# Kernel tuning notes

Hardware: AMD Instinct MI355X
Metric: run time of the kernel (lower is better)

## Reference

```python
import jax, jax.numpy as jnp
import numpy as np

N_NODES = 50000
N_EDGES = 800000
N_GRAPHS = 512
D_IN = 64
D_HID = 64
D_CLS = 128
LEAKY_SLOPE = 0.01


def _glorot(key, shape):
    fan_in, fan_out = shape[0], shape[1]
    lim = jnp.sqrt(6.0 / (fan_in + fan_out)).astype(jnp.float32)
    return jax.random.uniform(key, shape, jnp.float32, -lim, lim)


def setup_inputs() -> dict:
    key = jax.random.key(0)
    ks = jax.random.split(key, 16)
    x = jax.random.normal(ks[0], (N_NODES, D_IN), jnp.float32)
    edge_index = jax.random.randint(ks[1], (2, N_EDGES), 0, N_NODES, jnp.int32)
    batch = jnp.sort(jax.random.randint(ks[2], (N_NODES,), 0, N_GRAPHS, jnp.int32))
    return {
        'x': x,
        'W0': _glorot(ks[3], (D_IN, D_HID)), 'b0': jnp.zeros((D_HID,), jnp.float32),
        'W1': _glorot(ks[4], (D_HID, D_HID)), 'b1': jnp.zeros((D_HID,), jnp.float32),
        'W2': _glorot(ks[5], (D_HID, D_HID)), 'b2': jnp.zeros((D_HID,), jnp.float32),
        'lin1_w': _glorot(ks[6], (D_HID, D_CLS)), 'lin1_b': jnp.zeros((D_CLS,), jnp.float32),
        'lin2_w': _glorot(ks[7], (D_CLS, 1)), 'lin2_b': jnp.zeros((1,), jnp.float32),
        'fc_w': _glorot(ks[8], (1, 1)), 'fc_b': jnp.zeros((1,), jnp.float32),
        'edge_index': edge_index,
        'batch': batch,
    }


def _gcn_layer(h_in, W, b, src, dst, edge_norm, deg_inv):
    # GCNConv: linear transform, then symmetric-normalized aggregation with self-loops
    h = h_in @ W                                        # [N, D]
    msgs = h[src] * edge_norm[:, None]                  # gather + scale, [E, D]
    agg = jax.ops.segment_sum(msgs, dst, num_segments=N_NODES)  # scatter-add
    return agg + deg_inv[:, None] * h + b               # self-loop term + bias


def reference(x, W0, b0, W1, b1, W2, b2, lin1_w, lin1_b, lin2_w, lin2_b, fc_w, fc_b, edge_index, batch):
    src, dst = edge_index[0], edge_index[1]
    # degrees including self-loop (A + I)
    deg = jax.ops.segment_sum(jnp.ones((N_EDGES,), jnp.float32), dst, num_segments=N_NODES) + 1.0
    deg_inv_sqrt = jax.lax.rsqrt(deg)
    deg_inv = 1.0 / deg
    edge_norm = deg_inv_sqrt[src] * deg_inv_sqrt[dst]   # [E]

    h = _gcn_layer(x, W0, b0, src, dst, edge_norm, deg_inv)
    h = _gcn_layer(h, W1, b1, src, dst, edge_norm, deg_inv)
    h = _gcn_layer(h, W2, b2, src, dst, edge_norm, deg_inv)

    # global_mean_pool over graphs
    sums = jax.ops.segment_sum(h, batch, num_segments=N_GRAPHS)          # [G, D]
    counts = jax.ops.segment_sum(jnp.ones((N_NODES,), jnp.float32), batch, num_segments=N_GRAPHS)
    pooled = sums / jnp.maximum(counts, 1.0)[:, None]

    out = pooled @ lin1_w + lin1_b      # [G, cls_hidden]
    out = out @ lin2_w + lin2_b         # [G, 1]
    out = out @ fc_w + fc_b             # [G, 1]
    return jnp.where(out >= 0, out, LEAKY_SLOPE * out)  # LeakyReLU
```

## Files before the change

kernel.cpp:

```cpp
#include <hip/hip_runtime.h>
#include <math.h>

#define N_NODES 50000
#define N_EDGES 800000
#define N_GRAPHS 512
#define D 64
#define D_CLS 128
#define BNODES 128
#define NBUK 391
#define BSTRIDE 4096
#define PART_TILE 4096

typedef _Float16 h4 __attribute__((ext_vector_type(4)));
typedef float    f4 __attribute__((ext_vector_type(4)));

static inline int cdiv(int a, int b) { return (a + b - 1) / b; }


__global__ void k_binit(int* __restrict__ btail) {
    int b = blockIdx.x * blockDim.x + threadIdx.x;
    if (b < NBUK) btail[b] = b * BSTRIDE;
}


__global__ __launch_bounds__(256) void k_part(
        const int* __restrict__ src, const int* __restrict__ dst,
        int* __restrict__ btail, int* __restrict__ ebuf) {
    __shared__ int lcnt[NBUK];
    __shared__ int lbase[NBUK];
    int t = threadIdx.x;
    for (int i = t; i < NBUK; i += 256) lcnt[i] = 0;
    __syncthreads();

    int e0 = blockIdx.x * PART_TILE + t;
    int ent[16];
    int br[16];
    #pragma unroll
    for (int k = 0; k < 16; k++) {
        int e = e0 + k * 256;
        if (e < N_EDGES) {
            int d = dst[e];
            int b = d / BNODES;
            int r = atomicAdd(&lcnt[b], 1);
            ent[k] = src[e] | ((d & (BNODES - 1)) << 16);
            br[k] = (b << 16) | r;
        } else {
            br[k] = -1;
        }
    }
    __syncthreads();
    for (int i = t; i < NBUK; i += 256) {
        int c = lcnt[i];
        lbase[i] = c ? atomicAdd(&btail[i], c) : 0;
    }
    __syncthreads();
    #pragma unroll
    for (int k = 0; k < 16; k++) {
        if (br[k] >= 0) {
            int b = br[k] >> 16, r = br[k] & 0xFFFF;
            ebuf[lbase[b] + r] = ent[k];
        }
    }
}


__global__ __launch_bounds__(256) void k_build(
        const int* __restrict__ ebuf, const int* __restrict__ btail,
        int* __restrict__ rstart, int* __restrict__ rend,
        float* __restrict__ dis, int* __restrict__ col) {
    __shared__ int hist[BNODES];
    __shared__ int base[BNODES];
    __shared__ int cur[BNODES];
    int t = threadIdx.x;
    int b = blockIdx.x;
    int s = b * BSTRIDE;
    int e = btail[b];

    if (t < BNODES) { hist[t] = 0; cur[t] = 0; }
    __syncthreads();

    for (int i = s + t; i < e; i += 256)
        atomicAdd(&hist[(ebuf[i] >> 16) & (BNODES - 1)], 1);
    __syncthreads();

    if (t < BNODES) base[t] = hist[t];
    __syncthreads();
    for (int off = 1; off < BNODES; off <<= 1) {
        int x = 0;
        if (t < BNODES && t >= off) x = base[t - off];
        __syncthreads();
        if (t < BNODES) base[t] += x;
        __syncthreads();
    }
    if (t < BNODES) {
        int ex = base[t] - hist[t];
        base[t] = ex;
        int n = b * BNODES + t;
        if (n < N_NODES) {
            rstart[n] = s + ex;
            rend[n]   = s + ex + hist[t];
            dis[n] = rsqrtf((float)hist[t] + 1.0f);
        }
    }
    __syncthreads();

    for (int i = s + t; i < e; i += 256) {
        int v = ebuf[i];
        int d = (v >> 16) & (BNODES - 1);
        int pos = atomicAdd(&cur[d], 1);
        col[s + base[d] + pos] = v & 0xFFFF;
    }
}


#define XS_STRIDE 68

__global__ __launch_bounds__(256) void k_gemm_scale(
        const float* __restrict__ X, const float* __restrict__ W,
        const float* __restrict__ dis, _Float16* __restrict__ G16) {
    __shared__ float Xs[64 * XS_STRIDE];
    __shared__ float Ws[64 * 64];
    int n0 = blockIdx.x * 64;
    int t = threadIdx.x;

    {
        int base = t * 16;
        const float4* wsrc = (const float4*)(W + base);
        float4* wdst = (float4*)(Ws + base);
        wdst[0] = wsrc[0]; wdst[1] = wsrc[1]; wdst[2] = wsrc[2]; wdst[3] = wsrc[3];
    }
    {
        int row = t >> 2;
        int c0 = (t & 3) * 16;
        int grow = n0 + row;
        float4* xd = (float4*)(Xs + row * XS_STRIDE + c0);
        if (grow < N_NODES) {
            const float4* xp = (const float4*)(X + (size_t)grow * D + c0);
            xd[0] = xp[0]; xd[1] = xp[1]; xd[2] = xp[2]; xd[3] = xp[3];
        } else {
            float4 z = {0.f, 0.f, 0.f, 0.f};
            xd[0] = z; xd[1] = z; xd[2] = z; xd[3] = z;
        }
    }
    __syncthreads();

    int tc = t & 15, tr = t >> 4;
    int r0 = tr * 4, c0 = tc * 4;
    float acc[4][4] = {};
    #pragma unroll 4
    for (int k = 0; k < 64; k++) {
        float4 wv = *(const float4*)&Ws[k * 64 + c0];
        #pragma unroll
        for (int i = 0; i < 4; i++) {
            float xv = Xs[(r0 + i) * XS_STRIDE + k];
            acc[i][0] = fmaf(xv, wv.x, acc[i][0]);
            acc[i][1] = fmaf(xv, wv.y, acc[i][1]);
            acc[i][2] = fmaf(xv, wv.z, acc[i][2]);
            acc[i][3] = fmaf(xv, wv.w, acc[i][3]);
        }
    }
    #pragma unroll
    for (int i = 0; i < 4; i++) {
        int grow = n0 + r0 + i;
        if (grow < N_NODES) {
            float dsc = dis[grow];
            h4 o;
            o.x = (_Float16)(acc[i][0] * dsc);
            o.y = (_Float16)(acc[i][1] * dsc);
            o.z = (_Float16)(acc[i][2] * dsc);
            o.w = (_Float16)(acc[i][3] * dsc);
            *(h4*)&G16[(size_t)grow * D + c0] = o;
        }
    }
}


__global__ __launch_bounds__(256) void k_agg(
        const _Float16* __restrict__ G16, const int* __restrict__ rstart,
        const int* __restrict__ rend, const int* __restrict__ col,
        const float* __restrict__ dis, const float* __restrict__ bias,
        float* __restrict__ Out) {
    int t = threadIdx.x;
    int grp = t >> 4;
    int fl4 = (t & 15) * 4;
    int n = blockIdx.x * 16 + grp;

    int s = rstart[n], e = rend[n];
    f4 acc = __builtin_convertvector(*(const h4*)(G16 + (size_t)n * D + fl4), f4);

    for (int i = s; i < e; i += 8) {
        int i1 = i + 1, i2 = i + 2, i3 = i + 3;
        int i4 = i + 4, i5 = i + 5, i6 = i + 6, i7 = i + 7;
        int c0 = col[i];
        int c1 = col[i1 < e ? i1 : i];
        int c2 = col[i2 < e ? i2 : i];
        int c3 = col[i3 < e ? i3 : i];
        int c4 = col[i4 < e ? i4 : i];
        int c5 = col[i5 < e ? i5 : i];
        int c6 = col[i6 < e ? i6 : i];
        int c7 = col[i7 < e ? i7 : i];
        float f1 = (i1 < e) ? 1.f : 0.f;
        float f2 = (i2 < e) ? 1.f : 0.f;
        float f3 = (i3 < e) ? 1.f : 0.f;
        float f4_ = (i4 < e) ? 1.f : 0.f;
        float f5 = (i5 < e) ? 1.f : 0.f;
        float f6 = (i6 < e) ? 1.f : 0.f;
        float f7 = (i7 < e) ? 1.f : 0.f;
        f4 g0 = __builtin_convertvector(*(const h4*)(G16 + (size_t)c0 * D + fl4), f4);
        f4 g1 = __builtin_convertvector(*(const h4*)(G16 + (size_t)c1 * D + fl4), f4);
        f4 g2 = __builtin_convertvector(*(const h4*)(G16 + (size_t)c2 * D + fl4), f4);
        f4 g3 = __builtin_convertvector(*(const h4*)(G16 + (size_t)c3 * D + fl4), f4);
        f4 g4 = __builtin_convertvector(*(const h4*)(G16 + (size_t)c4 * D + fl4), f4);
        f4 g5 = __builtin_convertvector(*(const h4*)(G16 + (size_t)c5 * D + fl4), f4);
        f4 g6 = __builtin_convertvector(*(const h4*)(G16 + (size_t)c6 * D + fl4), f4);
        f4 g7 = __builtin_convertvector(*(const h4*)(G16 + (size_t)c7 * D + fl4), f4);
        acc += g0;
        acc += f1 * g1;
        acc += f2 * g2;
        acc += f3 * g3;
        acc += f4_ * g4;
        acc += f5 * g5;
        acc += f6 * g6;
        acc += f7 * g7;
    }

    float dsc = dis[n];
    f4 bv = *(const f4*)(bias + fl4);
    f4 o = dsc * acc + bv;
    *(f4*)(Out + (size_t)n * D + fl4) = o;
}


__device__ __forceinline__ int lower_bound_batch(const int* batch, int g) {
    int lo = 0, hi = N_NODES;
    while (lo < hi) {
        int mid = (lo + hi) >> 1;
        if (batch[mid] < g) lo = mid + 1; else hi = mid;
    }
    return lo;
}

__global__ __launch_bounds__(256) void k_pool(
        const float* __restrict__ H, const int* __restrict__ batch,
        float* __restrict__ P) {
    int g = blockIdx.x * 4 + (threadIdx.x >> 6);
    if (g >= N_GRAPHS) return;
    int lane = threadIdx.x & 63;
    int es  = lane >> 4;
    int fg4 = (lane & 15) * 4;
    int s = lower_bound_batch(batch, g);
    int e = lower_bound_batch(batch, g + 1);
    float4 acc = {0.f, 0.f, 0.f, 0.f};
    for (int r = s + es; r < e; r += 4) {
        float4 h = *(const float4*)(H + (size_t)r * D + fg4);
        acc.x += h.x; acc.y += h.y; acc.z += h.z; acc.w += h.w;
    }
    #pragma unroll
    for (int m = 16; m < 64; m <<= 1) {
        acc.x += __shfl_xor(acc.x, m, 64);
        acc.y += __shfl_xor(acc.y, m, 64);
        acc.z += __shfl_xor(acc.z, m, 64);
        acc.w += __shfl_xor(acc.w, m, 64);
    }
    int cntr = e - s;
    float inv = 1.0f / (float)(cntr > 0 ? cntr : 1);
    if (es == 0) {
        float4 o;
        o.x = acc.x * inv; o.y = acc.y * inv; o.z = acc.z * inv; o.w = acc.w * inv;
        *(float4*)(P + g * D + fg4) = o;
    }
}


__global__ __launch_bounds__(128) void k_mlp(
        const float* __restrict__ P,
        const float* __restrict__ w1, const float* __restrict__ b1,
        const float* __restrict__ w2, const float* __restrict__ b2,
        const float* __restrict__ fcw, const float* __restrict__ fcb,
        float* __restrict__ out) {
    __shared__ float ps[64];
    __shared__ float red[128];
    int g = blockIdx.x, t = threadIdx.x;
    if (t < 64) ps[t] = P[g * D + t];
    __syncthreads();
    float acc = b1[t];
    #pragma unroll
    for (int k = 0; k < 64; k++) acc = fmaf(ps[k], w1[k * D_CLS + t], acc);
    red[t] = acc * w2[t];
    __syncthreads();
    for (int s2 = 64; s2 > 0; s2 >>= 1) {
        if (t < s2) red[t] += red[t + s2];
        __syncthreads();
    }
    if (t == 0) {
        float o = red[0] + b2[0];
        o = fmaf(o, fcw[0], fcb[0]);
        out[g] = (o >= 0.f) ? o : 0.01f * o;
    }
}


extern "C" void kernel_launch(void* const* d_in, const int* in_sizes, int n_in,
                              void* d_out, int out_size, void* d_ws, size_t ws_size,
                              hipStream_t stream) {
    const float* x   = (const float*)d_in[0];
    const float* W0  = (const float*)d_in[1];
    const float* b0  = (const float*)d_in[2];
    const float* W1  = (const float*)d_in[3];
    const float* b1  = (const float*)d_in[4];
    const float* W2  = (const float*)d_in[5];
    const float* b2  = (const float*)d_in[6];
    const float* l1w = (const float*)d_in[7];
    const float* l1b = (const float*)d_in[8];
    const float* l2w = (const float*)d_in[9];
    const float* l2b = (const float*)d_in[10];
    const float* fcw = (const float*)d_in[11];
    const float* fcb = (const float*)d_in[12];
    const int* eidx  = (const int*)d_in[13];
    const int* batch = (const int*)d_in[14];
    const int* src = eidx;
    const int* dst = eidx + N_EDGES;

    char* ws = (char*)d_ws;
    size_t off = 0;
    auto alloc = [&](size_t bytes) -> void* {
        off = (off + 255) & ~(size_t)255;
        void* p = ws + off;
        off += bytes;
        return p;
    };

    int*   rstart = (int*)  alloc(N_NODES * sizeof(int));
    int*   rend   = (int*)  alloc(N_NODES * sizeof(int));
    int*   btail  = (int*)  alloc(NBUK * sizeof(int));
    int*   ebuf   = (int*)  alloc((size_t)NBUK * BSTRIDE * sizeof(int));
    int*   col    = (int*)  alloc((size_t)NBUK * BSTRIDE * sizeof(int));
    float* dis    = (float*)alloc(N_NODES * sizeof(float));
    _Float16* G16 = (_Float16*)alloc((size_t)N_NODES * D * sizeof(_Float16));
    float* bufB   = (float*)alloc((size_t)N_NODES * D * sizeof(float));
    float* bufC   = (float*)alloc((size_t)N_NODES * D * sizeof(float));
    float* pooled = (float*)alloc((size_t)N_GRAPHS * D * sizeof(float));

    const int nbPart = cdiv(N_EDGES, PART_TILE);

    k_binit<<<cdiv(NBUK, 256), 256, 0, stream>>>(btail);
    k_part<<<nbPart, 256, 0, stream>>>(src, dst, btail, ebuf);
    k_build<<<NBUK, 256, 0, stream>>>(ebuf, btail, rstart, rend, dis, col);

    const int nbGemm = cdiv(N_NODES, 64);
    const int nbAgg  = cdiv(N_NODES, 16);

    k_gemm_scale<<<nbGemm, 256, 0, stream>>>(x, W0, dis, G16);
    k_agg<<<nbAgg, 256, 0, stream>>>(G16, rstart, rend, col, dis, b0, bufB);
    k_gemm_scale<<<nbGemm, 256, 0, stream>>>(bufB, W1, dis, G16);
    k_agg<<<nbAgg, 256, 0, stream>>>(G16, rstart, rend, col, dis, b1, bufC);
    k_gemm_scale<<<nbGemm, 256, 0, stream>>>(bufC, W2, dis, G16);
    k_agg<<<nbAgg, 256, 0, stream>>>(G16, rstart, rend, col, dis, b2, bufB);

    k_pool<<<cdiv(N_GRAPHS, 4), 256, 0, stream>>>(bufB, batch, pooled);
    k_mlp<<<N_GRAPHS, 128, 0, stream>>>(pooled, l1w, l1b, l2w, l2b, fcw, fcb,
                                        (float*)d_out);
}
```

Measured before the change: 143.7 us.

## Store intermediate node features in fp16, fuse pooling into MLP, stage CSR build in LDS

Aggregation outputs are now written as fp16 and the next GEMM reads fp16 input, which halves the intermediate activation traffic between layers. Mean pooling is fused into the MLP kernel, removing one launch and the pooled buffer. The CSR build kernel stages its bucket in shared memory so the edge buffer is read from global memory once instead of twice. The cost is extra fp16 rounding of the hidden activations, and a pooling step now spread over 512 blocks of only 128 threads with narrow scalar loads.

Result: slower. 148.6 us (+3.4%).

```diff
diff --git a/kernel.cpp b/kernel.cpp
--- a/kernel.cpp
+++ b/kernel.cpp
@@ -68,19 +68,23 @@
         const int* __restrict__ ebuf, const int* __restrict__ btail,
         int* __restrict__ rstart, int* __restrict__ rend,
         float* __restrict__ dis, int* __restrict__ col) {
+    __shared__ int stage[BSTRIDE];
     __shared__ int hist[BNODES];
     __shared__ int base[BNODES];
     __shared__ int cur[BNODES];
     int t = threadIdx.x;
     int b = blockIdx.x;
     int s = b * BSTRIDE;
-    int e = btail[b];
+    int m = btail[b] - s;
 
     if (t < BNODES) { hist[t] = 0; cur[t] = 0; }
     __syncthreads();
 
-    for (int i = s + t; i < e; i += 256)
-        atomicAdd(&hist[(ebuf[i] >> 16) & (BNODES - 1)], 1);
+    for (int i = t; i < m; i += 256) {
+        int v = ebuf[s + i];
+        stage[i] = v;
+        atomicAdd(&hist[(v >> 16) & (BNODES - 1)], 1);
+    }
     __syncthreads();
 
     if (t < BNODES) base[t] = hist[t];
@@ -104,8 +108,8 @@
     }
     __syncthreads();
 
-    for (int i = s + t; i < e; i += 256) {
-        int v = ebuf[i];
+    for (int i = t; i < m; i += 256) {
+        int v = stage[i];
         int d = (v >> 16) & (BNODES - 1);
         int pos = atomicAdd(&cur[d], 1);
         col[s + base[d] + pos] = v & 0xFFFF;
@@ -115,8 +119,9 @@
 
 #define XS_STRIDE 68
 
+template<bool HALF_IN>
 __global__ __launch_bounds__(256) void k_gemm_scale(
-        const float* __restrict__ X, const float* __restrict__ W,
+        const void* __restrict__ Xv, const float* __restrict__ W,
         const float* __restrict__ dis, _Float16* __restrict__ G16) {
     __shared__ float Xs[64 * XS_STRIDE];
     __shared__ float Ws[64 * 64];
@@ -133,13 +138,22 @@
         int row = t >> 2;
         int c0 = (t & 3) * 16;
         int grow = n0 + row;
-        float4* xd = (float4*)(Xs + row * XS_STRIDE + c0);
+        float* xd = Xs + row * XS_STRIDE + c0;
         if (grow < N_NODES) {
-            const float4* xp = (const float4*)(X + (size_t)grow * D + c0);
-            xd[0] = xp[0]; xd[1] = xp[1]; xd[2] = xp[2]; xd[3] = xp[3];
+            if (HALF_IN) {
+                const h4* xp = (const h4*)((const _Float16*)Xv + (size_t)grow * D + c0);
+                #pragma unroll
+                for (int j = 0; j < 4; j++)
+                    *(f4*)(xd + j * 4) = __builtin_convertvector(xp[j], f4);
+            } else {
+                const float4* xp = (const float4*)((const float*)Xv + (size_t)grow * D + c0);
+                float4* xd4 = (float4*)xd;
+                xd4[0] = xp[0]; xd4[1] = xp[1]; xd4[2] = xp[2]; xd4[3] = xp[3];
+            }
         } else {
             float4 z = {0.f, 0.f, 0.f, 0.f};
-            xd[0] = z; xd[1] = z; xd[2] = z; xd[3] = z;
+            float4* xd4 = (float4*)xd;
+            xd4[0] = z; xd4[1] = z; xd4[2] = z; xd4[3] = z;
         }
     }
     __syncthreads();
@@ -179,7 +193,7 @@
         const _Float16* __restrict__ G16, const int* __restrict__ rstart,
         const int* __restrict__ rend, const int* __restrict__ col,
         const float* __restrict__ dis, const float* __restrict__ bias,
-        float* __restrict__ Out) {
+        _Float16* __restrict__ Hout) {
     int t = threadIdx.x;
     int grp = t >> 4;
     int fl4 = (t & 15) * 4;
@@ -227,7 +241,10 @@
     float dsc = dis[n];
     f4 bv = *(const f4*)(bias + fl4);
     f4 o = dsc * acc + bv;
-    *(f4*)(Out + (size_t)n * D + fl4) = o;
+    h4 oh;
+    oh.x = (_Float16)o.x; oh.y = (_Float16)o.y;
+    oh.z = (_Float16)o.z; oh.w = (_Float16)o.w;
+    *(h4*)(Hout + (size_t)n * D + fl4) = oh;
 }
 
 
@@ -240,40 +257,8 @@
     return lo;
 }
 
-__global__ __launch_bounds__(256) void k_pool(
-        const float* __restrict__ H, const int* __restrict__ batch,
-        float* __restrict__ P) {
-    int g = blockIdx.x * 4 + (threadIdx.x >> 6);
-    if (g >= N_GRAPHS) return;
-    int lane = threadIdx.x & 63;
-    int es  = lane >> 4;
-    int fg4 = (lane & 15) * 4;
-    int s = lower_bound_batch(batch, g);
-    int e = lower_bound_batch(batch, g + 1);
-    float4 acc = {0.f, 0.f, 0.f, 0.f};
-    for (int r = s + es; r < e; r += 4) {
-        float4 h = *(const float4*)(H + (size_t)r * D + fg4);
-        acc.x += h.x; acc.y += h.y; acc.z += h.z; acc.w += h.w;
-    }
-    #pragma unroll
-    for (int m = 16; m < 64; m <<= 1) {
-        acc.x += __shfl_xor(acc.x, m, 64);
-        acc.y += __shfl_xor(acc.y, m, 64);
-        acc.z += __shfl_xor(acc.z, m, 64);
-        acc.w += __shfl_xor(acc.w, m, 64);
-    }
-    int cntr = e - s;
-    float inv = 1.0f / (float)(cntr > 0 ? cntr : 1);
-    if (es == 0) {
-        float4 o;
-        o.x = acc.x * inv; o.y = acc.y * inv; o.z = acc.z * inv; o.w = acc.w * inv;
-        *(float4*)(P + g * D + fg4) = o;
-    }
-}
-
-
-__global__ __launch_bounds__(128) void k_mlp(
-        const float* __restrict__ P,
+__global__ __launch_bounds__(128) void k_poolmlp(
+        const _Float16* __restrict__ H16, const int* __restrict__ batch,
         const float* __restrict__ w1, const float* __restrict__ b1,
         const float* __restrict__ w2, const float* __restrict__ b2,
         const float* __restrict__ fcw, const float* __restrict__ fcb,
@@ -281,12 +266,25 @@
     __shared__ float ps[64];
     __shared__ float red[128];
     int g = blockIdx.x, t = threadIdx.x;
-    if (t < 64) ps[t] = P[g * D + t];
-    __syncthreads();
-    float acc = b1[t];
+    int s = lower_bound_batch(batch, g);
+    int e = lower_bound_batch(batch, g + 1);
+
+    int f = t & 63, slot = t >> 6;
+    float acc = 0.f;
+    for (int r = s + slot; r < e; r += 2)
+        acc += (float)H16[(size_t)r * D + f];
+    red[t] = acc;
+    __syncthreads();
+    if (t < 64) {
+        int cnt = e - s;
+        ps[t] = (red[t] + red[t + 64]) / (float)(cnt > 0 ? cnt : 1);
+    }
+    __syncthreads();
+
+    float a = b1[t];
     #pragma unroll
-    for (int k = 0; k < 64; k++) acc = fmaf(ps[k], w1[k * D_CLS + t], acc);
-    red[t] = acc * w2[t];
+    for (int k = 0; k < 64; k++) a = fmaf(ps[k], w1[k * D_CLS + t], a);
+    red[t] = a * w2[t];
     __syncthreads();
     for (int s2 = 64; s2 > 0; s2 >>= 1) {
         if (t < s2) red[t] += red[t + s2];
@@ -337,9 +335,8 @@
     int*   col    = (int*)  alloc((size_t)NBUK * BSTRIDE * sizeof(int));
     float* dis    = (float*)alloc(N_NODES * sizeof(float));
     _Float16* G16 = (_Float16*)alloc((size_t)N_NODES * D * sizeof(_Float16));
-    float* bufB   = (float*)alloc((size_t)N_NODES * D * sizeof(float));
-    float* bufC   = (float*)alloc((size_t)N_NODES * D * sizeof(float));
-    float* pooled = (float*)alloc((size_t)N_GRAPHS * D * sizeof(float));
+    _Float16* H1  = (_Float16*)alloc((size_t)N_NODES * D * sizeof(_Float16));
+    _Float16* H2  = (_Float16*)alloc((size_t)N_NODES * D * sizeof(_Float16));
 
     const int nbPart = cdiv(N_EDGES, PART_TILE);
 
@@ -350,14 +347,13 @@
     const int nbGemm = cdiv(N_NODES, 64);
     const int nbAgg  = cdiv(N_NODES, 16);
 
-    k_gemm_scale<<<nbGemm, 256, 0, stream>>>(x, W0, dis, G16);
-    k_agg<<<nbAgg, 256, 0, stream>>>(G16, rstart, rend, col, dis, b0, bufB);
-    k_gemm_scale<<<nbGemm, 256, 0, stream>>>(bufB, W1, dis, G16);
-    k_agg<<<nbAgg, 256, 0, stream>>>(G16, rstart, rend, col, dis, b1, bufC);
-    k_gemm_scale<<<nbGemm, 256, 0, stream>>>(bufC, W2, dis, G16);
-    k_agg<<<nbAgg, 256, 0, stream>>>(G16, rstart, rend, col, dis, b2, bufB);
-
-    k_pool<<<cdiv(N_GRAPHS, 4), 256, 0, stream>>>(bufB, batch, pooled);
-    k_mlp<<<N_GRAPHS, 128, 0, stream>>>(pooled, l1w, l1b, l2w, l2b, fcw, fcb,
-                                        (float*)d_out);
-}
+    k_gemm_scale<false><<<nbGemm, 256, 0, stream>>>(x, W0, dis, G16);
+    k_agg<<<nbAgg, 256, 0, stream>>>(G16, rstart, rend, col, dis, b0, H1);
+    k_gemm_scale<true><<<nbGemm, 256, 0, stream>>>(H1, W1, dis, G16);
+    k_agg<<<nbAgg, 256, 0, stream>>>(G16, rstart, rend, col, dis, b1, H2);
+    k_gemm_scale<true><<<nbGemm, 256, 0, stream>>>(H2, W2, dis, G16);
+    k_agg<<<nbAgg, 256, 0, stream>>>(G16, rstart, rend, col, dis, b2, H1);
+
+    k_poolmlp<<<N_GRAPHS, 128, 0, stream>>>(H1, batch, l1w, l1b, l2w, l2b,
+                                            fcw, fcb, (float*)d_out);
+}
```
